# Kernel optimization log

Hardware: AMD Instinct MI355X
Metric: run time of the kernel (lower is better)

## Reference

```python
import jax, jax.numpy as jnp
import numpy as np

N, E, EP, D = 50000, 600000, 200000, 128
L = 3  # gnn layers


def _w(k, shape):
    # Kaiming-ish init: scale by 1/sqrt(fan_in)
    return jax.random.normal(k, shape, jnp.float32) / jnp.sqrt(jnp.float32(shape[-2]))


def setup_inputs() -> dict:
    key = jax.random.key(0)
    ks = jax.random.split(key, 20)
    x = jax.random.normal(ks[0], (N, D), jnp.float32)
    edge_attr = jax.random.normal(ks[1], (E, 1), jnp.float32)
    edge_index = jax.random.randint(ks[2], (2, E), 0, N, jnp.int64)
    predict_edge_index = jax.random.randint(ks[3], (2, EP), 0, N, jnp.int64)
    return {
        "x": x,
        "edge_attr": edge_attr,
        "edge_index": edge_index,
        "predict_edge_index": predict_edge_index,
        # SAGEConv params per layer: out = lin_l(mean_aggr) + lin_r(x); lin_r has no bias
        "Wl": _w(ks[4], (L, D, D)),
        "bl": jnp.zeros((L, D), jnp.float32),
        "Wr": _w(ks[5], (L, D, D)),
        # edge update MLPs: layer0 in=2D+1, layers 1..L-1 in=3D
        "euW0": _w(ks[6], (2 * D + 1, D)),
        "euB0": jnp.zeros((D,), jnp.float32),
        "euW": _w(ks[7], (L - 1, 3 * D, D)),
        "euB": jnp.zeros((L - 1, D), jnp.float32),
        # node post MLP
        "pW1": _w(ks[8], (D, D)), "pb1": jnp.zeros((D,), jnp.float32),
        "pW2": _w(ks[9], (D, D)), "pb2": jnp.zeros((D,), jnp.float32),
        # edge predict MLP (predict_mode=0: concat of two node embeddings)
        "qW1": _w(ks[10], (2 * D, D)), "qb1": jnp.zeros((D,), jnp.float32),
        "qW2": _w(ks[11], (D, 1)), "qb2": jnp.zeros((1,), jnp.float32),
    }


def reference(x, edge_attr, edge_index, predict_edge_index,
              Wl, bl, Wr, euW0, euB0, euW, euB,
              pW1, pb1, pW2, pb2, qW1, qb1, qW2, qb2):
    # dropout p=0.0 / eval mode -> identity
    src, dst = edge_index[0], edge_index[1]
    n = x.shape[0]
    deg = jax.ops.segment_sum(jnp.ones(src.shape, jnp.float32), dst, num_segments=n)
    deg = jnp.maximum(deg, 1.0)[:, None]
    for l in range(L):
        # SAGEConv: mean-aggregate source features at destinations
        aggr = jax.ops.segment_sum(x[src], dst, num_segments=n) / deg
        x = jax.nn.relu(aggr @ Wl[l] + bl[l] + x @ Wr[l])
        # edge update: gather endpoints, concat with edge_attr, Linear+ReLU (+outer relu no-op)
        cat = jnp.concatenate([x[src], x[dst], edge_attr], axis=-1)
        if l == 0:
            edge_attr = jax.nn.relu(cat @ euW0 + euB0)
        else:
            edge_attr = jax.nn.relu(cat @ euW[l - 1] + euB[l - 1])
    # node post MLP
    x = jax.nn.relu(x @ pW1 + pb1) @ pW2 + pb2
    # predict_mode=0: gather pair endpoints and score
    xi = x[predict_edge_index[0]]
    xj = x[predict_edge_index[1]]
    h = jnp.concatenate([xi, xj], axis=-1)
    y = jax.nn.relu(h @ qW1 + qb1) @ qW2 + qb2  # [EP, 1]
    return y
```

## Files before the change

kernel.cpp:

```cpp
#include <hip/hip_runtime.h>


typedef __attribute__((ext_vector_type(8))) short bf16x8;
typedef __attribute__((ext_vector_type(4))) float f32x4;

__device__ __forceinline__ unsigned short f2bf(float x) {
  unsigned u = __float_as_uint(x);
  u += 0x7fffu + ((u >> 16) & 1u);
  return (unsigned short)(u >> 16);
}
__device__ __forceinline__ float bf2f(unsigned short h) {
  return __uint_as_float(((unsigned)h) << 16);
}
__device__ __forceinline__ float lo16f(unsigned u) { return __uint_as_float(u << 16); }
__device__ __forceinline__ float hi16f(unsigned u) { return __uint_as_float(u & 0xffff0000u); }

__device__ __forceinline__ void gload_lds16(const void* g, void* l) {
  __builtin_amdgcn_global_load_lds(
      (const __attribute__((address_space(1))) unsigned int*)g,
      (__attribute__((address_space(3))) unsigned int*)l, 16, 0, 0);
}

__global__ void k_count(const int* __restrict__ dst, int* __restrict__ cnt, int E) {
  int i = blockIdx.x * blockDim.x + threadIdx.x;
  if (i < E) atomicAdd(&cnt[dst[i]], 1);
}

__global__ void k_scan1(const int* __restrict__ cnt, int* __restrict__ rs,
                        float* __restrict__ degf, int* __restrict__ bsum, int n) {
  __shared__ int wsum[16];
  __shared__ int wpre[16];
  const int tid = threadIdx.x;
  const int lane = tid & 63;
  const int wv = tid >> 6;
  int i = blockIdx.x * 1024 + tid;
  int v = (i < n) ? cnt[i] : 0;
  int s = v;
#pragma unroll
  for (int off = 1; off < 64; off <<= 1) {
    int t = __shfl_up(s, off);
    if (lane >= off) s += t;
  }
  if (lane == 63) wsum[wv] = s;
  __syncthreads();
  if (tid < 16) {
    int t = wsum[tid];
    int ss = t;
#pragma unroll
    for (int off = 1; off < 16; off <<= 1) {
      int u = __shfl_up(ss, off);
      if (tid >= off) ss += u;
    }
    wpre[tid] = ss - t;
  }
  __syncthreads();
  if (i < n) {
    rs[i] = s - v + wpre[wv];
    degf[i] = (float)(v > 0 ? v : 1);
  }
  if (tid == 1023) bsum[blockIdx.x] = wpre[15] + wsum[15];
}

__global__ void k_scan3(int* __restrict__ rs, const int* __restrict__ bsum,
                        int* __restrict__ cursor, int n, int nb) {
  __shared__ int boff_s[64];
  __shared__ int total_s;
  int tid = threadIdx.x;
  if (tid < 64) {
    int v = (tid < nb) ? bsum[tid] : 0;
    int s = v;
#pragma unroll
    for (int off = 1; off < 64; off <<= 1) {
      int t = __shfl_up(s, off);
      if (tid >= off) s += t;
    }
    boff_s[tid] = s - v;
    if (tid == 63) total_s = s;
  }
  __syncthreads();
  int i = blockIdx.x * blockDim.x + tid;
  if (i < n) {
    int r = rs[i] + boff_s[i >> 10];
    rs[i] = r;
    cursor[i] = r;
  }
  if (blockIdx.x == 0 && tid == 0) rs[n] = total_s;
}

__global__ void k_scatter(const int* __restrict__ src, const int* __restrict__ dst,
                          int* __restrict__ cursor, int* __restrict__ csr, int E) {
  int i = blockIdx.x * blockDim.x + threadIdx.x;
  if (i < E) {
    int p = atomicAdd(&cursor[dst[i]], 1);
    csr[p] = src[i];
  }
}

__global__ void k_split(const float* __restrict__ x, unsigned* __restrict__ X,
                        long n2) {
  long g = (long)blockIdx.x * blockDim.x + threadIdx.x;
  if (g >= n2) return;
  float2 v = ((const float2*)x)[g];
  unsigned short hx = f2bf(v.x), hy = f2bf(v.y);
  unsigned short lx = f2bf(v.x - bf2f(hx)), ly = f2bf(v.y - bf2f(hy));
  long row = g >> 6, p = g & 63;
  X[row * 128 + p] = (unsigned)hx | ((unsigned)hy << 16);
  X[row * 128 + 64 + p] = (unsigned)lx | ((unsigned)ly << 16);
}

__global__ void k_packAll(const float* __restrict__ Wl, const float* __restrict__ Wr,
                          const float* __restrict__ pW1, const float* __restrict__ pW2,
                          const float* __restrict__ qW1,
                          unsigned short* __restrict__ hi,
                          unsigned short* __restrict__ lo) {
  int gid = blockIdx.x * blockDim.x + threadIdx.x;
  if (gid >= 10 * 2048) return;
  int mat = gid >> 11;
  const float* Wm;
  if (mat < 3) Wm = Wl + (size_t)mat * 16384;
  else if (mat < 6) Wm = Wr + (size_t)(mat - 3) * 16384;
  else if (mat == 6) Wm = pW1;
  else if (mat == 7) Wm = pW2;
  else Wm = qW1 + (size_t)(mat - 8) * 16384;
  int lane = gid & 63;
  int f = (gid >> 6) & 31;
  int nt = f >> 2, ks = f & 3;
  int nn = nt * 16 + (lane & 15);
  int k0 = ks * 32 + 8 * (lane >> 4);
  size_t dst = (size_t)gid * 8;
#pragma unroll
  for (int r = 0; r < 8; ++r) {
    float w = Wm[(size_t)(k0 + r) * 128 + nn];
    unsigned short h = f2bf(w);
    hi[dst + r] = h;
    lo[dst + r] = f2bf(w - bf2f(h));
  }
}

__device__ __forceinline__ void mm3term(f32x4 acc[8], const bf16x8 a_h[4],
                                        const bf16x8 a_l[4],
                                        const unsigned short* smh,
                                        const unsigned short* sml, int lane) {
#pragma unroll
  for (int ks = 0; ks < 4; ++ks)
#pragma unroll
    for (int nt = 0; nt < 8; ++nt) {
      const bf16x8 b_h = *(const bf16x8*)(smh + (nt * 4 + ks) * 512 + lane * 8);
      const bf16x8 b_l = *(const bf16x8*)(sml + (nt * 4 + ks) * 512 + lane * 8);
      acc[nt] = __builtin_amdgcn_mfma_f32_16x16x32_bf16(b_h, a_h[ks], acc[nt], 0, 0, 0);
      acc[nt] = __builtin_amdgcn_mfma_f32_16x16x32_bf16(b_h, a_l[ks], acc[nt], 0, 0, 0);
      acc[nt] = __builtin_amdgcn_mfma_f32_16x16x32_bf16(b_l, a_h[ks], acc[nt], 0, 0, 0);
    }
}

template <bool RELU>
__device__ __forceinline__ void t_store(const f32x4 acc[8], const float* bias,
                                        unsigned short* tw, int r16, int cq) {
#pragma unroll
  for (int nt = 0; nt < 8; ++nt) {
    int col = nt * 16 + cq;
    float4 bv = *(const float4*)(bias + col);
    float v0 = acc[nt][0] + bv.x, v1 = acc[nt][1] + bv.y;
    float v2 = acc[nt][2] + bv.z, v3 = acc[nt][3] + bv.w;
    if (RELU) {
      v0 = fmaxf(v0, 0.f); v1 = fmaxf(v1, 0.f);
      v2 = fmaxf(v2, 0.f); v3 = fmaxf(v3, 0.f);
    }
    unsigned short h0 = f2bf(v0), h1 = f2bf(v1), h2 = f2bf(v2), h3 = f2bf(v3);
    uint2 oh, ol;
    oh.x = (unsigned)h0 | ((unsigned)h1 << 16);
    oh.y = (unsigned)h2 | ((unsigned)h3 << 16);
    ol.x = (unsigned)f2bf(v0 - bf2f(h0)) | ((unsigned)f2bf(v1 - bf2f(h1)) << 16);
    ol.y = (unsigned)f2bf(v2 - bf2f(h2)) | ((unsigned)f2bf(v3 - bf2f(h3)) << 16);
    int idx = (r16 * 128 + col) ^ ((r16 & 7) << 3);
    *(uint2*)(tw + idx) = oh;
    *(uint2*)(tw + 2048 + idx) = ol;
  }
}

__device__ __forceinline__ void t_load(bf16x8 a_h[4], bf16x8 a_l[4],
                                       const unsigned short* tw, int r16, int kgrp) {
#pragma unroll
  for (int ks = 0; ks < 4; ++ks) {
    int idx = (r16 * 128 + ks * 32 + kgrp) ^ ((r16 & 7) << 3);
    a_h[ks] = *(const bf16x8*)(tw + idx);
    a_l[ks] = *(const bf16x8*)(tw + 2048 + idx);
  }
}

__global__ __launch_bounds__(512, 4) void k_layer(
    const unsigned short* __restrict__ Xin,
    const int* __restrict__ csr, const int* __restrict__ rs,
    const float* __restrict__ degf,
    const unsigned short* __restrict__ W0h, const unsigned short* __restrict__ W0l,
    const unsigned short* __restrict__ W1h, const unsigned short* __restrict__ W1l,
    const float* __restrict__ bias, unsigned short* __restrict__ Xout, int nrows) {
  __shared__ unsigned short smem[32768];
  unsigned short* smh = smem;
  unsigned short* sml = smem + 16384;

  const int tid = threadIdx.x;
  const int lane = tid & 63;
  const int wv = tid >> 6;
  const long row0 = ((long)blockIdx.x * 8 + wv) * 16;
  const bool active = row0 < nrows;
  const int r16 = lane & 15;
  const int kgrp = (lane >> 4) * 8;
  long rr = row0 + r16;
  const long arow = (rr < nrows) ? rr : (long)(nrows - 1);

#pragma unroll
  for (int k = 0; k < 4; ++k) {
    int t = tid + k * 512;
    gload_lds16((const uint4*)W0h + t, (uint4*)smh + t);
    gload_lds16((const uint4*)W0l + t, (uint4*)sml + t);
  }

  float am[4][8];
#pragma unroll
  for (int ks = 0; ks < 4; ++ks)
#pragma unroll
    for (int d = 0; d < 8; ++d) am[ks][d] = 0.f;

  bf16x8 a0h[4];
  if (active) {
    int s = rs[arow], e = rs[arow + 1];
    int j = s;
    for (; j + 1 < e; j += 2) {
      int n0 = csr[j], n1 = csr[j + 1];
      const unsigned short* b0 = Xin + (size_t)n0 * 256 + kgrp;
      const unsigned short* b1 = Xin + (size_t)n1 * 256 + kgrp;
#pragma unroll
      for (int ks = 0; ks < 4; ++ks) {
        uint4 v0 = *(const uint4*)(b0 + ks * 32);
        uint4 v1 = *(const uint4*)(b1 + ks * 32);
        am[ks][0] += lo16f(v0.x) + lo16f(v1.x);
        am[ks][1] += hi16f(v0.x) + hi16f(v1.x);
        am[ks][2] += lo16f(v0.y) + lo16f(v1.y);
        am[ks][3] += hi16f(v0.y) + hi16f(v1.y);
        am[ks][4] += lo16f(v0.z) + lo16f(v1.z);
        am[ks][5] += hi16f(v0.z) + hi16f(v1.z);
        am[ks][6] += lo16f(v0.w) + lo16f(v1.w);
        am[ks][7] += hi16f(v0.w) + hi16f(v1.w);
      }
    }
    if (j < e) {
      int n0 = csr[j];
      const unsigned short* b0 = Xin + (size_t)n0 * 256 + kgrp;
#pragma unroll
      for (int ks = 0; ks < 4; ++ks) {
        uint4 v0 = *(const uint4*)(b0 + ks * 32);
        am[ks][0] += lo16f(v0.x); am[ks][1] += hi16f(v0.x);
        am[ks][2] += lo16f(v0.y); am[ks][3] += hi16f(v0.y);
        am[ks][4] += lo16f(v0.z); am[ks][5] += hi16f(v0.z);
        am[ks][6] += lo16f(v0.w); am[ks][7] += hi16f(v0.w);
      }
    }
    float inv = 1.0f / degf[arow];
#pragma unroll
    for (int ks = 0; ks < 4; ++ks) {
      uint4 p;
      p.x = (unsigned)f2bf(am[ks][0] * inv) | ((unsigned)f2bf(am[ks][1] * inv) << 16);
      p.y = (unsigned)f2bf(am[ks][2] * inv) | ((unsigned)f2bf(am[ks][3] * inv) << 16);
      p.z = (unsigned)f2bf(am[ks][4] * inv) | ((unsigned)f2bf(am[ks][5] * inv) << 16);
      p.w = (unsigned)f2bf(am[ks][6] * inv) | ((unsigned)f2bf(am[ks][7] * inv) << 16);
      union { uint4 u; bf16x8 b; } cvt;
      cvt.u = p;
      a0h[ks] = cvt.b;
    }
  }

  bf16x8 a1h[4], a1l[4];
  if (active) {
#pragma unroll
    for (int ks = 0; ks < 4; ++ks) {
      a1h[ks] = *(const bf16x8*)(Xin + arow * 256 + ks * 32 + kgrp);
      a1l[ks] = *(const bf16x8*)(Xin + arow * 256 + 128 + ks * 32 + kgrp);
    }
  }

  f32x4 zero = {0.f, 0.f, 0.f, 0.f};
  f32x4 acc[8];
#pragma unroll
  for (int t = 0; t < 8; ++t) acc[t] = zero;

  __syncthreads();

  if (active) {
#pragma unroll
    for (int ks = 0; ks < 4; ++ks)
#pragma unroll
      for (int nt = 0; nt < 8; ++nt) {
        const bf16x8 b_h = *(const bf16x8*)(smh + (nt * 4 + ks) * 512 + lane * 8);
        const bf16x8 b_l = *(const bf16x8*)(sml + (nt * 4 + ks) * 512 + lane * 8);
        acc[nt] = __builtin_amdgcn_mfma_f32_16x16x32_bf16(b_h, a0h[ks], acc[nt], 0, 0, 0);
        acc[nt] = __builtin_amdgcn_mfma_f32_16x16x32_bf16(b_l, a0h[ks], acc[nt], 0, 0, 0);
      }
  }

  __syncthreads();
#pragma unroll
  for (int k = 0; k < 4; ++k) {
    int t = tid + k * 512;
    gload_lds16((const uint4*)W1h + t, (uint4*)smh + t);
    gload_lds16((const uint4*)W1l + t, (uint4*)sml + t);
  }
  __syncthreads();
  if (!active) return;

  mm3term(acc, a1h, a1l, smh, sml, lane);

  const int cq = (lane >> 4) * 4;
  const long row = row0 + r16;
  if (row >= nrows) return;
#pragma unroll
  for (int nt = 0; nt < 8; ++nt) {
    const int col = nt * 16 + cq;
    float4 bv = *(const float4*)(bias + col);
    float v0 = fmaxf(acc[nt][0] + bv.x, 0.f);
    float v1 = fmaxf(acc[nt][1] + bv.y, 0.f);
    float v2 = fmaxf(acc[nt][2] + bv.z, 0.f);
    float v3 = fmaxf(acc[nt][3] + bv.w, 0.f);
    unsigned short h0 = f2bf(v0), h1 = f2bf(v1), h2 = f2bf(v2), h3 = f2bf(v3);
    uint2 oh, ol;
    oh.x = (unsigned)h0 | ((unsigned)h1 << 16);
    oh.y = (unsigned)h2 | ((unsigned)h3 << 16);
    ol.x = (unsigned)f2bf(v0 - bf2f(h0)) | ((unsigned)f2bf(v1 - bf2f(h1)) << 16);
    ol.y = (unsigned)f2bf(v2 - bf2f(h2)) | ((unsigned)f2bf(v3 - bf2f(h3)) << 16);
    *(uint2*)(Xout + row * 256 + col) = oh;
    *(uint2*)(Xout + row * 256 + 128 + col) = ol;
  }
}

__global__ __launch_bounds__(512, 2) void k_post(
    const unsigned short* __restrict__ X,
    const unsigned short* __restrict__ W1h, const unsigned short* __restrict__ W1l,
    const unsigned short* __restrict__ W2h, const unsigned short* __restrict__ W2l,
    const unsigned short* __restrict__ W3h, const unsigned short* __restrict__ W3l,
    const unsigned short* __restrict__ W4h, const unsigned short* __restrict__ W4l,
    const float* __restrict__ b1, const float* __restrict__ b2,
    const float* __restrict__ b3, const float* __restrict__ b4,
    unsigned short* __restrict__ U, unsigned short* __restrict__ V, int nrows) {
  __shared__ unsigned short smem[32768];
  unsigned short* smh = smem;
  unsigned short* sml = smem + 16384;

  const int tid = threadIdx.x;
  const int lane = tid & 63;
  const int wv = tid >> 6;
  const long row0 = ((long)blockIdx.x * 8 + wv) * 16;
  const bool active = row0 < nrows;
  const int kgrp = (lane >> 4) * 8;
  const int r16 = lane & 15;
  const int cq = (lane >> 4) * 4;
  unsigned short* tw = smem + wv * 4096;

  long rr = row0 + r16;
  const long arow = (rr < nrows) ? rr : (long)(nrows - 1);
  const long row = row0 + r16;

#pragma unroll
  for (int k = 0; k < 4; ++k) {
    int t = tid + k * 512;
    gload_lds16((const uint4*)W1h + t, (uint4*)smh + t);
    gload_lds16((const uint4*)W1l + t, (uint4*)sml + t);
  }
  bf16x8 a_h[4], a_l[4];
  if (active) {
#pragma unroll
    for (int ks = 0; ks < 4; ++ks) {
      a_h[ks] = *(const bf16x8*)(X + arow * 256 + ks * 32 + kgrp);
      a_l[ks] = *(const bf16x8*)(X + arow * 256 + 128 + ks * 32 + kgrp);
    }
  }
  f32x4 zero = {0.f, 0.f, 0.f, 0.f};
  f32x4 acc[8];
#pragma unroll
  for (int t = 0; t < 8; ++t) acc[t] = zero;

  __syncthreads();
  if (active) mm3term(acc, a_h, a_l, smh, sml, lane);
  __syncthreads();

  if (active) {
    t_store<true>(acc, b1, tw, r16, cq);
    t_load(a_h, a_l, tw, r16, kgrp);
  }
  __syncthreads();

#pragma unroll
  for (int k = 0; k < 4; ++k) {
    int t = tid + k * 512;
    gload_lds16((const uint4*)W2h + t, (uint4*)smh + t);
    gload_lds16((const uint4*)W2l + t, (uint4*)sml + t);
  }
#pragma unroll
  for (int t = 0; t < 8; ++t) acc[t] = zero;
  __syncthreads();
  if (active) mm3term(acc, a_h, a_l, smh, sml, lane);
  __syncthreads();

  if (active) {
    t_store<false>(acc, b2, tw, r16, cq);
    t_load(a_h, a_l, tw, r16, kgrp);
  }
  __syncthreads();

#pragma unroll
  for (int k = 0; k < 4; ++k) {
    int t = tid + k * 512;
    gload_lds16((const uint4*)W3h + t, (uint4*)smh + t);
    gload_lds16((const uint4*)W3l + t, (uint4*)sml + t);
  }
#pragma unroll
  for (int t = 0; t < 8; ++t) acc[t] = zero;
  __syncthreads();
  if (active) mm3term(acc, a_h, a_l, smh, sml, lane);
  if (active && row < nrows) {
#pragma unroll
    for (int nt = 0; nt < 8; ++nt) {
      const int col = nt * 16 + cq;
      float4 bv = *(const float4*)(b3 + col);
      unsigned short h0 = f2bf(acc[nt][0] + bv.x), h1 = f2bf(acc[nt][1] + bv.y);
      unsigned short h2 = f2bf(acc[nt][2] + bv.z), h3 = f2bf(acc[nt][3] + bv.w);
      uint2 oh;
      oh.x = (unsigned)h0 | ((unsigned)h1 << 16);
      oh.y = (unsigned)h2 | ((unsigned)h3 << 16);
      *(uint2*)(U + row * 128 + col) = oh;
    }
  }
  __syncthreads();

#pragma unroll
  for (int k = 0; k < 4; ++k) {
    int t = tid + k * 512;
    gload_lds16((const uint4*)W4h + t, (uint4*)smh + t);
    gload_lds16((const uint4*)W4l + t, (uint4*)sml + t);
  }
#pragma unroll
  for (int t = 0; t < 8; ++t) acc[t] = zero;
  __syncthreads();
  if (!active || row >= nrows) return;
  mm3term(acc, a_h, a_l, smh, sml, lane);
#pragma unroll
  for (int nt = 0; nt < 8; ++nt) {
    const int col = nt * 16 + cq;
    float4 bv = *(const float4*)(b4 + col);
    unsigned short h0 = f2bf(acc[nt][0] + bv.x), h1 = f2bf(acc[nt][1] + bv.y);
    unsigned short h2 = f2bf(acc[nt][2] + bv.z), h3 = f2bf(acc[nt][3] + bv.w);
    uint2 oh;
    oh.x = (unsigned)h0 | ((unsigned)h1 << 16);
    oh.y = (unsigned)h2 | ((unsigned)h3 << 16);
    *(uint2*)(V + row * 128 + col) = oh;
  }
}

__global__ __launch_bounds__(256) void k_pair(
    const unsigned short* __restrict__ u, const unsigned short* __restrict__ v,
    const int* __restrict__ ps, const int* __restrict__ pd,
    const float* __restrict__ qW2, const float* __restrict__ qb2,
    float* __restrict__ out, int EP) {
  int gid = blockIdx.x * blockDim.x + threadIdx.x;
  long wid = gid >> 6;
  int lane = gid & 63;
  int sub = lane & 15, g = lane >> 4;
  long base = wid * 8;
  if (base >= EP) return;
  float4 q0 = *(const float4*)(qW2 + sub * 8);
  float4 q1 = *(const float4*)(qW2 + sub * 8 + 4);
  float qb = qb2[0];

  long p0 = base + g;
  long p1 = base + 4 + g;
  long c0 = (p0 < EP) ? p0 : (EP - 1);
  long c1 = (p1 < EP) ? p1 : (EP - 1);
  int i0 = ps[c0], j0 = pd[c0];
  int i1 = ps[c1], j1 = pd[c1];
  uint4 a0 = *(const uint4*)(u + (size_t)i0 * 128 + sub * 8);
  uint4 b0 = *(const uint4*)(v + (size_t)j0 * 128 + sub * 8);
  uint4 a1 = *(const uint4*)(u + (size_t)i1 * 128 + sub * 8);
  uint4 b1 = *(const uint4*)(v + (size_t)j1 * 128 + sub * 8);

  float s0, s1;
  {
    float t;
    t = fmaxf(lo16f(a0.x) + lo16f(b0.x), 0.f) * q0.x;
    t = fmaf(fmaxf(hi16f(a0.x) + hi16f(b0.x), 0.f), q0.y, t);
    t = fmaf(fmaxf(lo16f(a0.y) + lo16f(b0.y), 0.f), q0.z, t);
    t = fmaf(fmaxf(hi16f(a0.y) + hi16f(b0.y), 0.f), q0.w, t);
    t = fmaf(fmaxf(lo16f(a0.z) + lo16f(b0.z), 0.f), q1.x, t);
    t = fmaf(fmaxf(hi16f(a0.z) + hi16f(b0.z), 0.f), q1.y, t);
    t = fmaf(fmaxf(lo16f(a0.w) + lo16f(b0.w), 0.f), q1.z, t);
    t = fmaf(fmaxf(hi16f(a0.w) + hi16f(b0.w), 0.f), q1.w, t);
    s0 = t;
    t = fmaxf(lo16f(a1.x) + lo16f(b1.x), 0.f) * q0.x;
    t = fmaf(fmaxf(hi16f(a1.x) + hi16f(b1.x), 0.f), q0.y, t);
    t = fmaf(fmaxf(lo16f(a1.y) + lo16f(b1.y), 0.f), q0.z, t);
    t = fmaf(fmaxf(hi16f(a1.y) + hi16f(b1.y), 0.f), q0.w, t);
    t = fmaf(fmaxf(lo16f(a1.z) + lo16f(b1.z), 0.f), q1.x, t);
    t = fmaf(fmaxf(hi16f(a1.z) + hi16f(b1.z), 0.f), q1.y, t);
    t = fmaf(fmaxf(lo16f(a1.w) + lo16f(b1.w), 0.f), q1.z, t);
    t = fmaf(fmaxf(hi16f(a1.w) + hi16f(b1.w), 0.f), q1.w, t);
    s1 = t;
  }
#pragma unroll
  for (int m = 1; m < 16; m <<= 1) {
    s0 += __shfl_xor(s0, m);
    s1 += __shfl_xor(s1, m);
  }
  if (sub == 0) {
    if (p0 < EP) out[p0] = s0 + qb;
    if (p1 < EP) out[p1] = s1 + qb;
  }
}

extern "C" void kernel_launch(void* const* d_in, const int* in_sizes, int n_in,
                              void* d_out, int out_size, void* d_ws, size_t ws_size,
                              hipStream_t stream) {
  const float* x_in = (const float*)d_in[0];
  const int* ei = (const int*)d_in[2];
  const int* pe = (const int*)d_in[3];
  const float* Wl = (const float*)d_in[4];
  const float* bl = (const float*)d_in[5];
  const float* Wr = (const float*)d_in[6];
  const float* pW1 = (const float*)d_in[11];
  const float* pb1 = (const float*)d_in[12];
  const float* pW2 = (const float*)d_in[13];
  const float* pb2 = (const float*)d_in[14];
  const float* qW1 = (const float*)d_in[15];
  const float* qb1 = (const float*)d_in[16];
  const float* qW2 = (const float*)d_in[17];
  const float* qb2 = (const float*)d_in[18];

  const int N = in_sizes[0] / 128;
  const int E = in_sizes[2] / 2;
  const int EP = in_sizes[3] / 2;
  const int* e_src = ei;
  const int* e_dst = ei + E;
  const int* p_src = pe;
  const int* p_dst = pe + EP;

  char* ws = (char*)d_ws;
  size_t off = 0;
  auto alloc = [&](size_t bytes) {
    void* p = ws + off;
    off += (bytes + 511) & ~(size_t)511;
    return p;
  };
  unsigned short* X0 = (unsigned short*)alloc((size_t)N * 256 * 2);
  unsigned short* X1 = (unsigned short*)alloc((size_t)N * 256 * 2);
  int* deg_i = (int*)alloc((size_t)N * 4);
  int* rs = (int*)alloc((size_t)(N + 1) * 4);
  int* cursor = (int*)alloc((size_t)N * 4);
  float* degf = (float*)alloc((size_t)N * 4);
  int* csr = (int*)alloc((size_t)E * 4);
  int* bsum = (int*)alloc(64 * 4);
  unsigned short* Whi = (unsigned short*)alloc((size_t)10 * 16384 * 2);
  unsigned short* Wlo = (unsigned short*)alloc((size_t)10 * 16384 * 2);
  float* zerob = (float*)alloc(128 * 4);

  const size_t MS = 16384;
  const int nb = (N + 1023) / 1024;

  hipMemsetAsync(deg_i, 0, (size_t)N * 4, stream);
  hipMemsetAsync(zerob, 0, 128 * 4, stream);

  k_packAll<<<(10 * 2048 + 255) / 256, 256, 0, stream>>>(Wl, Wr, pW1, pW2, qW1,
                                                         Whi, Wlo);

  long n2 = (long)N * 64;
  k_split<<<(int)((n2 + 255) / 256), 256, 0, stream>>>(x_in, (unsigned*)X0, n2);

  k_count<<<(E + 255) / 256, 256, 0, stream>>>(e_dst, deg_i, E);
  k_scan1<<<nb, 1024, 0, stream>>>(deg_i, rs, degf, bsum, N);
  k_scan3<<<(N + 255) / 256, 256, 0, stream>>>(rs, bsum, cursor, N, nb);
  k_scatter<<<(E + 255) / 256, 256, 0, stream>>>(e_src, e_dst, cursor, csr, E);

  const int gmm = (N + 127) / 128;

  unsigned short* Xi = X0;
  unsigned short* Xo = X1;
  for (int l = 0; l < 3; ++l) {
    k_layer<<<gmm, 512, 0, stream>>>(
        Xi, csr, rs, degf, Whi + (size_t)l * MS, Wlo + (size_t)l * MS,
        Whi + (size_t)(3 + l) * MS, Wlo + (size_t)(3 + l) * MS,
        bl + (size_t)l * 128, Xo, N);
    unsigned short* t = Xi; Xi = Xo; Xo = t;
  }
  unsigned short* u = Xo;
  unsigned short* v = Xo + (size_t)N * 128;
  k_post<<<gmm, 512, 0, stream>>>(
      Xi, Whi + 6 * MS, Wlo + 6 * MS, Whi + 7 * MS, Wlo + 7 * MS,
      Whi + 8 * MS, Wlo + 8 * MS, Whi + 9 * MS, Wlo + 9 * MS,
      pb1, pb2, qb1, zerob, u, v, N);
  k_pair<<<(EP + 31) / 32, 256, 0, stream>>>(u, v, p_src, p_dst, qW2, qb2,
                                             (float*)d_out, EP);
}
```

Measured before the change: 282.6 us.

## Halve k_layer LDS by streaming weight matrices in two column halves

The layer kernel now stages each 128x128 weight matrix (hi and lo bf16 parts) in LDS as two 64-column halves instead of whole, cutting shared memory per block from 64KB to 32KB. The launch bound's blocks-per-CU hint rises from 4 to 6 to exploit the freed LDS. The goal is more resident blocks so the irregular neighbor gather latency is better hidden. In exchange it adds extra barriers and serialized weight loads between half-matmuls, and the higher occupancy target may cap registers and cause spills.

```diff
diff --git a/kernel.cpp b/kernel.cpp
--- a/kernel.cpp
+++ b/kernel.cpp
@@ -137,6 +137,43 @@
   }
 }
 
+__device__ __forceinline__ void mm2half(f32x4 acc[8], const bf16x8 a_h[4],
+                                        const unsigned short* smh,
+                                        const unsigned short* sml, int lane,
+                                        int half) {
+#pragma unroll
+  for (int ks = 0; ks < 4; ++ks)
+#pragma unroll
+    for (int ntl = 0; ntl < 4; ++ntl) {
+      const bf16x8 b_h = *(const bf16x8*)(smh + (ntl * 4 + ks) * 512 + lane * 8);
+      const bf16x8 b_l = *(const bf16x8*)(sml + (ntl * 4 + ks) * 512 + lane * 8);
+      acc[half * 4 + ntl] =
+          __builtin_amdgcn_mfma_f32_16x16x32_bf16(b_h, a_h[ks], acc[half * 4 + ntl], 0, 0, 0);
+      acc[half * 4 + ntl] =
+          __builtin_amdgcn_mfma_f32_16x16x32_bf16(b_l, a_h[ks], acc[half * 4 + ntl], 0, 0, 0);
+    }
+}
+
+__device__ __forceinline__ void mm3half(f32x4 acc[8], const bf16x8 a_h[4],
+                                        const bf16x8 a_l[4],
+                                        const unsigned short* smh,
+                                        const unsigned short* sml, int lane,
+                                        int half) {
+#pragma unroll
+  for (int ks = 0; ks < 4; ++ks)
+#pragma unroll
+    for (int ntl = 0; ntl < 4; ++ntl) {
+      const bf16x8 b_h = *(const bf16x8*)(smh + (ntl * 4 + ks) * 512 + lane * 8);
+      const bf16x8 b_l = *(const bf16x8*)(sml + (ntl * 4 + ks) * 512 + lane * 8);
+      acc[half * 4 + ntl] =
+          __builtin_amdgcn_mfma_f32_16x16x32_bf16(b_h, a_h[ks], acc[half * 4 + ntl], 0, 0, 0);
+      acc[half * 4 + ntl] =
+          __builtin_amdgcn_mfma_f32_16x16x32_bf16(b_h, a_l[ks], acc[half * 4 + ntl], 0, 0, 0);
+      acc[half * 4 + ntl] =
+          __builtin_amdgcn_mfma_f32_16x16x32_bf16(b_l, a_h[ks], acc[half * 4 + ntl], 0, 0, 0);
+    }
+}
+
 __device__ __forceinline__ void mm3term(f32x4 acc[8], const bf16x8 a_h[4],
                                         const bf16x8 a_l[4],
                                         const unsigned short* smh,
@@ -188,16 +225,16 @@
   }
 }
 
-__global__ __launch_bounds__(512, 4) void k_layer(
+__global__ __launch_bounds__(512, 6) void k_layer(
     const unsigned short* __restrict__ Xin,
     const int* __restrict__ csr, const int* __restrict__ rs,
     const float* __restrict__ degf,
     const unsigned short* __restrict__ W0h, const unsigned short* __restrict__ W0l,
     const unsigned short* __restrict__ W1h, const unsigned short* __restrict__ W1l,
     const float* __restrict__ bias, unsigned short* __restrict__ Xout, int nrows) {
-  __shared__ unsigned short smem[32768];
+  __shared__ unsigned short smem[16384];
   unsigned short* smh = smem;
-  unsigned short* sml = smem + 16384;
+  unsigned short* sml = smem + 8192;
 
   const int tid = threadIdx.x;
   const int lane = tid & 63;
@@ -210,7 +247,7 @@
   const long arow = (rr < nrows) ? rr : (long)(nrows - 1);
 
 #pragma unroll
-  for (int k = 0; k < 4; ++k) {
+  for (int k = 0; k < 2; ++k) {
     int t = tid + k * 512;
     gload_lds16((const uint4*)W0h + t, (uint4*)smh + t);
     gload_lds16((const uint4*)W0l + t, (uint4*)sml + t);
@@ -285,30 +322,35 @@
   for (int t = 0; t < 8; ++t) acc[t] = zero;
 
   __syncthreads();
-
-  if (active) {
-#pragma unroll
-    for (int ks = 0; ks < 4; ++ks)
-#pragma unroll
-      for (int nt = 0; nt < 8; ++nt) {
-        const bf16x8 b_h = *(const bf16x8*)(smh + (nt * 4 + ks) * 512 + lane * 8);
-        const bf16x8 b_l = *(const bf16x8*)(sml + (nt * 4 + ks) * 512 + lane * 8);
-        acc[nt] = __builtin_amdgcn_mfma_f32_16x16x32_bf16(b_h, a0h[ks], acc[nt], 0, 0, 0);
-        acc[nt] = __builtin_amdgcn_mfma_f32_16x16x32_bf16(b_l, a0h[ks], acc[nt], 0, 0, 0);
-      }
-  }
-
-  __syncthreads();
-#pragma unroll
-  for (int k = 0; k < 4; ++k) {
+  if (active) mm2half(acc, a0h, smh, sml, lane, 0);
+  __syncthreads();
+#pragma unroll
+  for (int k = 0; k < 2; ++k) {
+    int t = tid + k * 512;
+    gload_lds16((const uint4*)W0h + 1024 + t, (uint4*)smh + t);
+    gload_lds16((const uint4*)W0l + 1024 + t, (uint4*)sml + t);
+  }
+  __syncthreads();
+  if (active) mm2half(acc, a0h, smh, sml, lane, 1);
+  __syncthreads();
+#pragma unroll
+  for (int k = 0; k < 2; ++k) {
     int t = tid + k * 512;
     gload_lds16((const uint4*)W1h + t, (uint4*)smh + t);
     gload_lds16((const uint4*)W1l + t, (uint4*)sml + t);
   }
   __syncthreads();
+  if (active) mm3half(acc, a1h, a1l, smh, sml, lane, 0);
+  __syncthreads();
+#pragma unroll
+  for (int k = 0; k < 2; ++k) {
+    int t = tid + k * 512;
+    gload_lds16((const uint4*)W1h + 1024 + t, (uint4*)smh + t);
+    gload_lds16((const uint4*)W1l + 1024 + t, (uint4*)sml + t);
+  }
+  __syncthreads();
   if (!active) return;
-
-  mm3term(acc, a1h, a1l, smh, sml, lane);
+  mm3half(acc, a1h, a1l, smh, sml, lane, 1);
 
   const int cq = (lane >> 4) * 4;
   const long row = row0 + r16;
```

Result: slower. 305.2 us (+8.0%).

## Renumber nodes by in-degree to balance aggregation work across waves

Applied to the files above, without the earlier changes.

Computes a counting-sort permutation of nodes by in-degree (descending) and relabels node rows, CSR sources and destinations, and pair indices through it. Rows handled by the same wave or block in the layer kernel then have similar neighbor counts, which reduces divergence and load imbalance in the gather-mean aggregation. In exchange it adds several small kernels (histogram, scan, position assignment, count permutation) and an extra indirection in the split, scatter and pair kernels. It also scatters the x rows on write and loses any locality that came from the original node order.

```diff
diff --git a/kernel.cpp b/kernel.cpp
--- a/kernel.cpp
+++ b/kernel.cpp
@@ -24,6 +24,62 @@
 __global__ void k_count(const int* __restrict__ dst, int* __restrict__ cnt, int E) {
   int i = blockIdx.x * blockDim.x + threadIdx.x;
   if (i < E) atomicAdd(&cnt[dst[i]], 1);
+}
+
+__global__ void k_hist(const int* __restrict__ cnt, int* __restrict__ hist, int n) {
+  int i = blockIdx.x * blockDim.x + threadIdx.x;
+  if (i < n) {
+    int b = cnt[i];
+    b = b < 1023 ? b : 1023;
+    atomicAdd(&hist[b], 1);
+  }
+}
+
+__global__ void k_hscan(const int* __restrict__ hist, int* __restrict__ hcur) {
+  __shared__ int wsum[16];
+  __shared__ int wpre[16];
+  const int tid = threadIdx.x;
+  const int lane = tid & 63;
+  const int wv = tid >> 6;
+  int v = hist[tid];
+  int s = v;
+#pragma unroll
+  for (int off = 1; off < 64; off <<= 1) {
+    int t = __shfl_up(s, off);
+    if (lane >= off) s += t;
+  }
+  if (lane == 63) wsum[wv] = s;
+  __syncthreads();
+  if (tid < 16) {
+    int t = wsum[tid];
+    int ss = t;
+#pragma unroll
+    for (int off = 1; off < 16; off <<= 1) {
+      int u = __shfl_up(ss, off);
+      if (tid >= off) ss += u;
+    }
+    wpre[tid] = ss - t;
+  }
+  __syncthreads();
+  int incl = s + wpre[wv];
+  int total = wpre[15] + wsum[15];
+  hcur[tid] = total - incl;
+}
+
+__global__ void k_permpos(const int* __restrict__ cnt, int* __restrict__ hcur,
+                          int* __restrict__ o2s, int n) {
+  int i = blockIdx.x * blockDim.x + threadIdx.x;
+  if (i < n) {
+    int b = cnt[i];
+    b = b < 1023 ? b : 1023;
+    o2s[i] = atomicAdd(&hcur[b], 1);
+  }
+}
+
+__global__ void k_permcnt(const int* __restrict__ cnt, const int* __restrict__ o2s,
+                          int* __restrict__ cnt2, int n) {
+  int i = blockIdx.x * blockDim.x + threadIdx.x;
+  if (i < n) cnt2[o2s[i]] = cnt[i];
 }
 
 __global__ void k_scan1(const int* __restrict__ cnt, int* __restrict__ rs,
@@ -88,24 +144,26 @@
 }
 
 __global__ void k_scatter(const int* __restrict__ src, const int* __restrict__ dst,
-                          int* __restrict__ cursor, int* __restrict__ csr, int E) {
+                          const int* __restrict__ o2s, int* __restrict__ cursor,
+                          int* __restrict__ csr, int E) {
   int i = blockIdx.x * blockDim.x + threadIdx.x;
   if (i < E) {
-    int p = atomicAdd(&cursor[dst[i]], 1);
-    csr[p] = src[i];
-  }
-}
-
-__global__ void k_split(const float* __restrict__ x, unsigned* __restrict__ X,
-                        long n2) {
+    int p = atomicAdd(&cursor[o2s[dst[i]]], 1);
+    csr[p] = o2s[src[i]];
+  }
+}
+
+__global__ void k_split(const float* __restrict__ x, const int* __restrict__ o2s,
+                        unsigned* __restrict__ X, long n2) {
   long g = (long)blockIdx.x * blockDim.x + threadIdx.x;
   if (g >= n2) return;
   float2 v = ((const float2*)x)[g];
   unsigned short hx = f2bf(v.x), hy = f2bf(v.y);
   unsigned short lx = f2bf(v.x - bf2f(hx)), ly = f2bf(v.y - bf2f(hy));
   long row = g >> 6, p = g & 63;
-  X[row * 128 + p] = (unsigned)hx | ((unsigned)hy << 16);
-  X[row * 128 + 64 + p] = (unsigned)lx | ((unsigned)ly << 16);
+  long srow = o2s[row];
+  X[srow * 128 + p] = (unsigned)hx | ((unsigned)hy << 16);
+  X[srow * 128 + 64 + p] = (unsigned)lx | ((unsigned)ly << 16);
 }
 
 __global__ void k_packAll(const float* __restrict__ Wl, const float* __restrict__ Wr,
@@ -458,6 +516,7 @@
 __global__ __launch_bounds__(256) void k_pair(
     const unsigned short* __restrict__ u, const unsigned short* __restrict__ v,
     const int* __restrict__ ps, const int* __restrict__ pd,
+    const int* __restrict__ o2s,
     const float* __restrict__ qW2, const float* __restrict__ qb2,
     float* __restrict__ out, int EP) {
   int gid = blockIdx.x * blockDim.x + threadIdx.x;
@@ -474,8 +533,8 @@
   long p1 = base + 4 + g;
   long c0 = (p0 < EP) ? p0 : (EP - 1);
   long c1 = (p1 < EP) ? p1 : (EP - 1);
-  int i0 = ps[c0], j0 = pd[c0];
-  int i1 = ps[c1], j1 = pd[c1];
+  int i0 = o2s[ps[c0]], j0 = o2s[pd[c0]];
+  int i1 = o2s[ps[c1]], j1 = o2s[pd[c1]];
   uint4 a0 = *(const uint4*)(u + (size_t)i0 * 128 + sub * 8);
   uint4 b0 = *(const uint4*)(v + (size_t)j0 * 128 + sub * 8);
   uint4 a1 = *(const uint4*)(u + (size_t)i1 * 128 + sub * 8);
@@ -550,31 +609,42 @@
   unsigned short* X0 = (unsigned short*)alloc((size_t)N * 256 * 2);
   unsigned short* X1 = (unsigned short*)alloc((size_t)N * 256 * 2);
   int* deg_i = (int*)alloc((size_t)N * 4);
+  int* cnt2 = (int*)alloc((size_t)N * 4);
+  int* o2s = (int*)alloc((size_t)N * 4);
   int* rs = (int*)alloc((size_t)(N + 1) * 4);
   int* cursor = (int*)alloc((size_t)N * 4);
   float* degf = (float*)alloc((size_t)N * 4);
   int* csr = (int*)alloc((size_t)E * 4);
   int* bsum = (int*)alloc(64 * 4);
+  int* hist = (int*)alloc(1024 * 4);
+  int* hcur = (int*)alloc(1024 * 4);
   unsigned short* Whi = (unsigned short*)alloc((size_t)10 * 16384 * 2);
   unsigned short* Wlo = (unsigned short*)alloc((size_t)10 * 16384 * 2);
   float* zerob = (float*)alloc(128 * 4);
 
   const size_t MS = 16384;
   const int nb = (N + 1023) / 1024;
+  const int nblk = (N + 255) / 256;
 
   hipMemsetAsync(deg_i, 0, (size_t)N * 4, stream);
+  hipMemsetAsync(hist, 0, 1024 * 4, stream);
   hipMemsetAsync(zerob, 0, 128 * 4, stream);
 
   k_packAll<<<(10 * 2048 + 255) / 256, 256, 0, stream>>>(Wl, Wr, pW1, pW2, qW1,
                                                          Whi, Wlo);
 
+  k_count<<<(E + 255) / 256, 256, 0, stream>>>(e_dst, deg_i, E);
+  k_hist<<<nblk, 256, 0, stream>>>(deg_i, hist, N);
+  k_hscan<<<1, 1024, 0, stream>>>(hist, hcur);
+  k_permpos<<<nblk, 256, 0, stream>>>(deg_i, hcur, o2s, N);
+  k_permcnt<<<nblk, 256, 0, stream>>>(deg_i, o2s, cnt2, N);
+
   long n2 = (long)N * 64;
-  k_split<<<(int)((n2 + 255) / 256), 256, 0, stream>>>(x_in, (unsigned*)X0, n2);
-
-  k_count<<<(E + 255) / 256, 256, 0, stream>>>(e_dst, deg_i, E);
-  k_scan1<<<nb, 1024, 0, stream>>>(deg_i, rs, degf, bsum, N);
-  k_scan3<<<(N + 255) / 256, 256, 0, stream>>>(rs, bsum, cursor, N, nb);
-  k_scatter<<<(E + 255) / 256, 256, 0, stream>>>(e_src, e_dst, cursor, csr, E);
+  k_split<<<(int)((n2 + 255) / 256), 256, 0, stream>>>(x_in, o2s, (unsigned*)X0, n2);
+
+  k_scan1<<<nb, 1024, 0, stream>>>(cnt2, rs, degf, bsum, N);
+  k_scan3<<<nblk, 256, 0, stream>>>(rs, bsum, cursor, N, nb);
+  k_scatter<<<(E + 255) / 256, 256, 0, stream>>>(e_src, e_dst, o2s, cursor, csr, E);
 
   const int gmm = (N + 127) / 128;
 
@@ -593,6 +663,6 @@
       Xi, Whi + 6 * MS, Wlo + 6 * MS, Whi + 7 * MS, Wlo + 7 * MS,
       Whi + 8 * MS, Wlo + 8 * MS, Whi + 9 * MS, Wlo + 9 * MS,
       pb1, pb2, qb1, zerob, u, v, N);
-  k_pair<<<(EP + 31) / 32, 256, 0, stream>>>(u, v, p_src, p_dst, qW2, qb2,
+  k_pair<<<(EP + 31) / 32, 256, 0, stream>>>(u, v, p_src, p_dst, o2s, qW2, qb2,
                                              (float*)d_out, EP);
 }
```

New measurement: 617.2 us. 118% more time.
